# Optimization experiments

Measured on AMD Instinct MI355X. Metric: run time of the kernel, lower is better.

The kernel has to match this reference:

```python
import jax, jax.numpy as jnp
import numpy as np

H = 200  # LSTM units per layer
SEQ_LEN = 100
NUM_AXIS = 4


def setup_inputs() -> dict:
    key = jax.random.key(0)
    ks = jax.random.split(key, 12)
    B = 8192
    s = 0.05  # small init scale to avoid gate saturation
    inp = {
        "x": jax.random.normal(ks[0], (B, SEQ_LEN, 1), dtype=jnp.float32),
        # layer 0: input dim 1
        "W0": jax.random.normal(ks[1], (1, 4 * H), dtype=jnp.float32) * s,
        "U0": jax.random.normal(ks[2], (H, 4 * H), dtype=jnp.float32) * s,
        "b0": jax.random.normal(ks[3], (4 * H,), dtype=jnp.float32) * s,
        # layer 1
        "W1": jax.random.normal(ks[4], (H, 4 * H), dtype=jnp.float32) * s,
        "U1": jax.random.normal(ks[5], (H, 4 * H), dtype=jnp.float32) * s,
        "b1": jax.random.normal(ks[6], (4 * H,), dtype=jnp.float32) * s,
        # layer 2
        "W2": jax.random.normal(ks[7], (H, 4 * H), dtype=jnp.float32) * s,
        "U2": jax.random.normal(ks[8], (H, 4 * H), dtype=jnp.float32) * s,
        "b2": jax.random.normal(ks[9], (4 * H,), dtype=jnp.float32) * s,
        # dense head: 200 -> 400, tanh
        "Wfc": jax.random.normal(ks[10], (H, SEQ_LEN * NUM_AXIS), dtype=jnp.float32) * s,
        "bfc": jax.random.normal(ks[11], (SEQ_LEN * NUM_AXIS,), dtype=jnp.float32) * s,
    }
    return inp


def _lstm_step(h, c, xt, W, U, b):
    # Keras LSTMCell gate order: i, f, g(candidate), o
    z = xt @ W + h @ U + b  # [B, 4H]
    i, f, g, o = jnp.split(z, 4, axis=-1)
    c_new = jax.nn.sigmoid(f) * c + jax.nn.sigmoid(i) * jnp.tanh(g)
    h_new = jax.nn.sigmoid(o) * jnp.tanh(c_new)
    return h_new, c_new


def reference(x, W0, U0, b0, W1, U1, b1, W2, U2, b2, Wfc, bfc):
    B = x.shape[0]
    zeros = jnp.zeros((B, H), dtype=x.dtype)
    carry0 = (zeros, zeros, zeros, zeros, zeros, zeros)

    def step(carry, xt):
        h0, c0, h1, c1, h2, c2 = carry
        h0, c0 = _lstm_step(h0, c0, xt, W0, U0, b0)
        h1, c1 = _lstm_step(h1, c1, h0, W1, U1, b1)
        h2, c2 = _lstm_step(h2, c2, h1, W2, U2, b2)
        return (h0, c0, h1, c1, h2, c2), None

    # scan over time: x is [B, T, 1] -> [T, B, 1]
    xs = jnp.swapaxes(x, 0, 1)
    (h0, c0, h1, c1, h2, c2), _ = jax.lax.scan(step, carry0, xs)
    # return_sequences=False -> final top-layer hidden state
    y = jnp.tanh(h2 @ Wfc + bfc)  # [B, 400]
    return y.reshape(B, SEQ_LEN, NUM_AXIS)
```

## Files before the change

### kernel.cpp

```cpp
#include <hip/hip_runtime.h>

#define Hdim 200
#define NP   800
#define Tlen 100
#define BT   32
#define KB   7
#define HS   232
#define NT   50
#define THREADS 640
#define CH   5
#define CHSTR (NT*64*8)
#define MATSZ (KB*CHSTR)
#define SBUF  2560

#define WAIT_VM0   0x0F70
#define WAIT_VM5   0x0F75
#define WAIT_LGKM0 0xC07F

typedef float f32x4 __attribute__((ext_vector_type(4)));
typedef short s16x8 __attribute__((ext_vector_type(8)));

__device__ __forceinline__ ushort f2bf(float f) {
    unsigned u = __float_as_uint(f);
    return (ushort)((u + 0x7fffu + ((u >> 16) & 1u)) >> 16);
}
__device__ __forceinline__ float bf2f(ushort s) {
    return __uint_as_float(((unsigned)s) << 16);
}
__device__ __forceinline__ float sigmoid_fast(float v) {
    return 1.0f / (1.0f + __expf(-v));
}
__device__ __forceinline__ float tanh_fast(float v) {
    return 2.0f / (1.0f + __expf(-2.0f * v)) - 1.0f;
}
__device__ __forceinline__ void wg_barrier() {
    asm volatile("" ::: "memory");
    __builtin_amdgcn_s_waitcnt(WAIT_LGKM0);
    __builtin_amdgcn_s_barrier();
    asm volatile("" ::: "memory");
}

__global__ void pack_weights(const float* __restrict__ U0, const float* __restrict__ W1,
                             const float* __restrict__ U1, const float* __restrict__ W2,
                             const float* __restrict__ U2, ushort* __restrict__ dst) {
    int idx = blockIdx.x * blockDim.x + threadIdx.x;
    if (idx >= 5 * KB * NT * 64) return;
    int lane = idx & 63; int rest = idx >> 6;
    int nt = rest % NT; rest /= NT;
    int kb = rest % KB; int mi = rest / KB;
    const float* src = (mi == 0) ? U0 : (mi == 1) ? W1 : (mi == 2) ? U1 : (mi == 3) ? W2 : U2;
    int np = nt * 16 + (lane & 15);
    int ncol = (np & 3) * Hdim + (np >> 2);
    int k0 = kb * 32 + (lane >> 4) * 8;
    ushort v[8];
#pragma unroll
    for (int j = 0; j < 8; ++j) {
        int k = k0 + j;
        v[j] = (k < Hdim) ? f2bf(src[k * NP + ncol]) : (ushort)0;
    }
    uint4 o;
    o.x = (unsigned)v[0] | ((unsigned)v[1] << 16);
    o.y = (unsigned)v[2] | ((unsigned)v[3] << 16);
    o.z = (unsigned)v[4] | ((unsigned)v[5] << 16);
    o.w = (unsigned)v[6] | ((unsigned)v[7] << 16);
    ((uint4*)dst)[idx] = o;
}

__device__ __forceinline__ void stage_chunk(const ushort* gp, ushort* dstbuf, int lane) {
#pragma unroll
    for (int mt = 0; mt < CH; ++mt) {
        __builtin_amdgcn_global_load_lds(
            (const __attribute__((address_space(1))) void*)(gp + (size_t)mt * 512 + lane * 8),
            (__attribute__((address_space(3))) void*)(dstbuf + mt * 512),
            16, 0, 0);
    }
}

__device__ __forceinline__ void unpack4(const ushort* p, float (&o)[4]) {
    uint2 u = *(const uint2*)p;
    o[0] = bf2f((ushort)(u.x));  o[1] = bf2f((ushort)(u.x >> 16));
    o[2] = bf2f((ushort)(u.y));  o[3] = bf2f((ushort)(u.y >> 16));
}

__device__ __forceinline__ void gate_phase(f32x4 (&acc)[2][CH],
                                           float (&creg)[2][CH],
                                           ushort* __restrict__ hbl,
                                           int lane, int ct0) {
    const int l15 = lane & 15, q = lane >> 4;
#pragma unroll
    for (int nt = 0; nt < 2; ++nt) {
#pragma unroll
        for (int mt = 0; mt < CH; ++mt) {
            const int u = (ct0 + mt) * 4 + q;
            const int n = nt * 16 + l15;
            f32x4 z = acc[nt][mt];
            float iv = sigmoid_fast(z[0]);
            float fv = sigmoid_fast(z[1]);
            float gv = tanh_fast(z[2]);
            float ov = sigmoid_fast(z[3]);
            float c = fv * creg[nt][mt] + iv * gv;
            creg[nt][mt] = c;
            hbl[n * HS + u] = f2bf(ov * tanh_fast(c));
        }
    }
}

__global__ void __launch_bounds__(THREADS)
lstm3_mfma(const float* __restrict__ x,
           const float* __restrict__ W0, const float* __restrict__ b0,
           const float* __restrict__ b1, const float* __restrict__ b2,
           const float* __restrict__ Wfc, const float* __restrict__ bfc,
           const ushort* __restrict__ packed,
           float* __restrict__ out) {
    __shared__ ushort hb[3][BT][HS];
    __shared__ ushort stage[10][2][SBUF];
    __shared__ ushort pbwb[4][NP];
    __shared__ ushort xTs[Tlen][BT];
    __shared__ uint   gTab[35];
    __shared__ uint   bhTab[35];

    const int tid = threadIdx.x;
    const int wave = tid >> 6, lane = tid & 63;
    const int l15 = lane & 15, q = lane >> 4;
    const int ct0 = wave * CH;
    const int bx = blockIdx.x;
    const int bbase = bx * BT;

    for (int i = tid; i < 3 * BT * HS; i += THREADS) ((ushort*)hb)[i] = 0;
    for (int i = tid; i < NP; i += THREADS) {
        int nc = (i & 3) * Hdim + (i >> 2);
        pbwb[0][i] = f2bf(b0[nc]); pbwb[1][i] = f2bf(b1[nc]);
        pbwb[2][i] = f2bf(b2[nc]); pbwb[3][i] = f2bf(W0[nc]);
    }
    for (int i = tid; i < BT * Tlen; i += THREADS) {
        int m = i / Tlen, tt = i % Tlen;
        xTs[tt][m] = f2bf(x[(size_t)(bbase + m) * Tlen + tt]);
    }
    if (tid < 35) {
        int s = tid; uint goff, bhoff;
        if (s < 7) {
            int c = (s + bx) % 7;
            goff = 0u * MATSZ + c * CHSTR;           bhoff = 0u * BT * HS + c * 32;
        } else if (s < 21) {
            int c = (s - 7 + bx) % 14;
            if (c < 7) { goff = 2u * MATSZ + c * CHSTR;       bhoff = 1u * BT * HS + c * 32; }
            else       { goff = 1u * MATSZ + (c - 7) * CHSTR; bhoff = 0u * BT * HS + (c - 7) * 32; }
        } else {
            int c = (s - 21 + bx * 5) % 14;
            if (c < 7) { goff = 4u * MATSZ + c * CHSTR;       bhoff = 2u * BT * HS + c * 32; }
            else       { goff = 3u * MATSZ + (c - 7) * CHSTR; bhoff = 1u * BT * HS + (c - 7) * 32; }
        }
        gTab[s] = goff; bhTab[s] = bhoff;
    }
    __syncthreads();

    float creg[3][2][CH];
#pragma unroll
    for (int l = 0; l < 3; ++l)
#pragma unroll
        for (int nt = 0; nt < 2; ++nt)
#pragma unroll
            for (int mt = 0; mt < CH; ++mt) creg[l][nt][mt] = 0.0f;

    const ushort* pk = packed + (size_t)(ct0 * 64) * 8;
    ushort* sl = &stage[wave][0][0];
    ushort* hbflat = &hb[0][0][0];
    const int bhbase = l15 * HS + q * 8;

    stage_chunk(pk + gTab[0], sl, lane);
    stage_chunk(pk + gTab[1], sl + SBUF, lane);
    int isl = 2;

    for (int t = 0; t < Tlen; ++t) {
        f32x4 acc[2][CH];

        const float xn0 = bf2f(xTs[t][l15]);
        const float xn1 = bf2f(xTs[t][16 + l15]);
#pragma unroll
        for (int mt = 0; mt < CH; ++mt) {
            const int row = (ct0 + mt) * 16 + q * 4;
            float bb[4], ww[4];
            unpack4(&pbwb[0][row], bb);
            unpack4(&pbwb[3][row], ww);
#pragma unroll
            for (int r = 0; r < 4; ++r) {
                acc[0][mt][r] = fmaf(xn0, ww[r], bb[r]);
                acc[1][mt][r] = fmaf(xn1, ww[r], bb[r]);
            }
        }

#pragma unroll 1
        for (int s = 0; s < 7; ++s) {
            __builtin_amdgcn_s_waitcnt(WAIT_VM5);
            ushort* buf = sl + ((t + s) & 1) * SBUF;
            s16x8 frag[CH];
#pragma unroll
            for (int mt = 0; mt < CH; ++mt)
                frag[mt] = *(const s16x8*)(buf + mt * 512 + lane * 8);
            const ushort* bp = hbflat + bhTab[s] + bhbase;
            s16x8 bh0 = *(const s16x8*)bp;
            s16x8 bh1 = *(const s16x8*)(bp + 16 * HS);
#pragma unroll
            for (int mt = 0; mt < CH; ++mt) {
                acc[0][mt] = __builtin_amdgcn_mfma_f32_16x16x32_bf16(frag[mt], bh0, acc[0][mt], 0, 0, 0);
                acc[1][mt] = __builtin_amdgcn_mfma_f32_16x16x32_bf16(frag[mt], bh1, acc[1][mt], 0, 0, 0);
            }
            __builtin_amdgcn_s_waitcnt(WAIT_LGKM0);
            stage_chunk(pk + gTab[isl], buf, lane);
            isl = (isl == 34) ? 0 : isl + 1;
        }
        wg_barrier();
        gate_phase(acc, creg[0], hbflat + 0 * BT * HS, lane, ct0);
        wg_barrier();

#pragma unroll
        for (int mt = 0; mt < CH; ++mt) {
            const int row = (ct0 + mt) * 16 + q * 4;
            float bb[4];
            unpack4(&pbwb[1][row], bb);
#pragma unroll
            for (int r = 0; r < 4; ++r) { acc[0][mt][r] = bb[r]; acc[1][mt][r] = bb[r]; }
        }
#pragma unroll 1
        for (int s = 7; s < 21; ++s) {
            __builtin_amdgcn_s_waitcnt(WAIT_VM5);
            ushort* buf = sl + ((t + s) & 1) * SBUF;
            s16x8 frag[CH];
#pragma unroll
            for (int mt = 0; mt < CH; ++mt)
                frag[mt] = *(const s16x8*)(buf + mt * 512 + lane * 8);
            const ushort* bp = hbflat + bhTab[s] + bhbase;
            s16x8 bh0 = *(const s16x8*)bp;
            s16x8 bh1 = *(const s16x8*)(bp + 16 * HS);
#pragma unroll
            for (int mt = 0; mt < CH; ++mt) {
                acc[0][mt] = __builtin_amdgcn_mfma_f32_16x16x32_bf16(frag[mt], bh0, acc[0][mt], 0, 0, 0);
                acc[1][mt] = __builtin_amdgcn_mfma_f32_16x16x32_bf16(frag[mt], bh1, acc[1][mt], 0, 0, 0);
            }
            __builtin_amdgcn_s_waitcnt(WAIT_LGKM0);
            stage_chunk(pk + gTab[isl], buf, lane);
            isl = (isl == 34) ? 0 : isl + 1;
        }
        wg_barrier();
        gate_phase(acc, creg[1], hbflat + 1 * BT * HS, lane, ct0);
        wg_barrier();

#pragma unroll
        for (int mt = 0; mt < CH; ++mt) {
            const int row = (ct0 + mt) * 16 + q * 4;
            float bb[4];
            unpack4(&pbwb[2][row], bb);
#pragma unroll
            for (int r = 0; r < 4; ++r) { acc[0][mt][r] = bb[r]; acc[1][mt][r] = bb[r]; }
        }
#pragma unroll 1
        for (int s = 21; s < 35; ++s) {
            __builtin_amdgcn_s_waitcnt(WAIT_VM5);
            ushort* buf = sl + ((t + s) & 1) * SBUF;
            s16x8 frag[CH];
#pragma unroll
            for (int mt = 0; mt < CH; ++mt)
                frag[mt] = *(const s16x8*)(buf + mt * 512 + lane * 8);
            const ushort* bp = hbflat + bhTab[s] + bhbase;
            s16x8 bh0 = *(const s16x8*)bp;
            s16x8 bh1 = *(const s16x8*)(bp + 16 * HS);
#pragma unroll
            for (int mt = 0; mt < CH; ++mt) {
                acc[0][mt] = __builtin_amdgcn_mfma_f32_16x16x32_bf16(frag[mt], bh0, acc[0][mt], 0, 0, 0);
                acc[1][mt] = __builtin_amdgcn_mfma_f32_16x16x32_bf16(frag[mt], bh1, acc[1][mt], 0, 0, 0);
            }
            __builtin_amdgcn_s_waitcnt(WAIT_LGKM0);
            stage_chunk(pk + gTab[isl], buf, lane);
            isl = (isl == 34) ? 0 : isl + 1;
        }
        wg_barrier();
        gate_phase(acc, creg[2], hbflat + 2 * BT * HS, lane, ct0);
        wg_barrier();
    }
    __syncthreads();

    for (int gidx = tid; gidx < BT * 100; gidx += THREADS) {
        int m = gidx / 100;
        int j4 = (gidx % 100) * 4;
        const ushort* h2 = &hb[2][m][0];
        float4 a4 = *(const float4*)(bfc + j4);
        float s0 = a4.x, s1 = a4.y, s2 = a4.z, s3 = a4.w;
        for (int k = 0; k < Hdim; ++k) {
            float hk = bf2f(h2[k]);
            float4 w4 = *(const float4*)(Wfc + (size_t)k * 400 + j4);
            s0 = fmaf(hk, w4.x, s0);
            s1 = fmaf(hk, w4.y, s1);
            s2 = fmaf(hk, w4.z, s2);
            s3 = fmaf(hk, w4.w, s3);
        }
        float4 o4;
        o4.x = tanh_fast(s0); o4.y = tanh_fast(s1);
        o4.z = tanh_fast(s2); o4.w = tanh_fast(s3);
        *(float4*)(out + (size_t)(bbase + m) * 400 + j4) = o4;
    }
}

extern "C" void kernel_launch(void* const* d_in, const int* in_sizes, int n_in,
                              void* d_out, int out_size, void* d_ws, size_t ws_size,
                              hipStream_t stream) {
    const float* x   = (const float*)d_in[0];
    const float* W0  = (const float*)d_in[1];
    const float* U0  = (const float*)d_in[2];
    const float* b0  = (const float*)d_in[3];
    const float* W1  = (const float*)d_in[4];
    const float* U1  = (const float*)d_in[5];
    const float* b1  = (const float*)d_in[6];
    const float* W2  = (const float*)d_in[7];
    const float* U2  = (const float*)d_in[8];
    const float* b2  = (const float*)d_in[9];
    const float* Wfc = (const float*)d_in[10];
    const float* bfc = (const float*)d_in[11];
    float* out = (float*)d_out;
    ushort* packed = (ushort*)d_ws;

    const int B = in_sizes[0] / Tlen;
    const int pack_threads = 5 * KB * NT * 64;
    pack_weights<<<(pack_threads + 255) / 256, 256, 0, stream>>>(U0, W1, U1, W2, U2, packed);
    lstm3_mfma<<<B / BT, THREADS, 0, stream>>>(x, W0, b0, b1, b2, Wfc, bfc, packed, out);
}
```

Measured before the change: 2.800 ms.

## Reorder LSTM matmul chunks to drop post-gate barriers per layer

Reorders the staged weight chunks so that each layer first multiplies against the hidden state of the layer whose fresh value is not yet needed. A barrier then sits between the two halves instead of after each gate phase, removing three workgroup barriers per timestep. The intent is to overlap the recurrent half of each matmul with other waves finishing their gate phase. It relies on careful reasoning about read-after-write hazards on the shared hidden buffers, which are now protected only by the reordered barriers.

Measured after the change: 2.840 ms. About the same (+1.4%).

```diff
diff --git a/kernel.cpp b/kernel.cpp
--- a/kernel.cpp
+++ b/kernel.cpp
@@ -13,7 +13,6 @@
 #define MATSZ (KB*CHSTR)
 #define SBUF  2560
 
-#define WAIT_VM0   0x0F70
 #define WAIT_VM5   0x0F75
 #define WAIT_LGKM0 0xC07F
 
@@ -82,6 +81,35 @@
     o[2] = bf2f((ushort)(u.y));  o[3] = bf2f((ushort)(u.y >> 16));
 }
 
+template<int S0, int S1>
+__device__ __forceinline__ void do_region(f32x4 (&acc)[2][CH],
+                                          const ushort* __restrict__ pk, ushort* sl,
+                                          const uint* __restrict__ gTab,
+                                          const uint* __restrict__ bhTab,
+                                          const ushort* __restrict__ hbflat,
+                                          int bhbase, int lane, int t, int& isl) {
+#pragma unroll 1
+    for (int s = S0; s < S1; ++s) {
+        __builtin_amdgcn_s_waitcnt(WAIT_VM5);
+        ushort* buf = sl + ((t + s) & 1) * SBUF;
+        s16x8 frag[CH];
+#pragma unroll
+        for (int mt = 0; mt < CH; ++mt)
+            frag[mt] = *(const s16x8*)(buf + mt * 512 + lane * 8);
+        const ushort* bp = hbflat + bhTab[s] + bhbase;
+        s16x8 bh0 = *(const s16x8*)bp;
+        s16x8 bh1 = *(const s16x8*)(bp + 16 * HS);
+#pragma unroll
+        for (int mt = 0; mt < CH; ++mt) {
+            acc[0][mt] = __builtin_amdgcn_mfma_f32_16x16x32_bf16(frag[mt], bh0, acc[0][mt], 0, 0, 0);
+            acc[1][mt] = __builtin_amdgcn_mfma_f32_16x16x32_bf16(frag[mt], bh1, acc[1][mt], 0, 0, 0);
+        }
+        __builtin_amdgcn_s_waitcnt(WAIT_LGKM0);
+        stage_chunk(pk + gTab[isl], buf, lane);
+        isl = (isl == 34) ? 0 : isl + 1;
+    }
+}
+
 __device__ __forceinline__ void gate_phase(f32x4 (&acc)[2][CH],
                                            float (&creg)[2][CH],
                                            ushort* __restrict__ hbl,
@@ -137,19 +165,13 @@
         xTs[tt][m] = f2bf(x[(size_t)(bbase + m) * Tlen + tt]);
     }
     if (tid < 35) {
-        int s = tid; uint goff, bhoff;
-        if (s < 7) {
-            int c = (s + bx) % 7;
-            goff = 0u * MATSZ + c * CHSTR;           bhoff = 0u * BT * HS + c * 32;
-        } else if (s < 21) {
-            int c = (s - 7 + bx) % 14;
-            if (c < 7) { goff = 2u * MATSZ + c * CHSTR;       bhoff = 1u * BT * HS + c * 32; }
-            else       { goff = 1u * MATSZ + (c - 7) * CHSTR; bhoff = 0u * BT * HS + (c - 7) * 32; }
-        } else {
-            int c = (s - 21 + bx * 5) % 14;
-            if (c < 7) { goff = 4u * MATSZ + c * CHSTR;       bhoff = 2u * BT * HS + c * 32; }
-            else       { goff = 3u * MATSZ + (c - 7) * CHSTR; bhoff = 1u * BT * HS + (c - 7) * 32; }
-        }
+        int s = tid; int r = s % 7; int c = (r + bx) % 7;
+        uint goff, bhoff;
+        if (s < 7)       { goff = 0u * MATSZ + c * CHSTR; bhoff = 0u * BT * HS + c * 32; }
+        else if (s < 14) { goff = 2u * MATSZ + c * CHSTR; bhoff = 1u * BT * HS + c * 32; }
+        else if (s < 21) { goff = 1u * MATSZ + c * CHSTR; bhoff = 0u * BT * HS + c * 32; }
+        else if (s < 28) { goff = 4u * MATSZ + c * CHSTR; bhoff = 2u * BT * HS + c * 32; }
+        else             { goff = 3u * MATSZ + c * CHSTR; bhoff = 1u * BT * HS + c * 32; }
         gTab[s] = goff; bhTab[s] = bhoff;
     }
     __syncthreads();
@@ -188,30 +210,9 @@
                 acc[1][mt][r] = fmaf(xn1, ww[r], bb[r]);
             }
         }
-
-#pragma unroll 1
-        for (int s = 0; s < 7; ++s) {
-            __builtin_amdgcn_s_waitcnt(WAIT_VM5);
-            ushort* buf = sl + ((t + s) & 1) * SBUF;
-            s16x8 frag[CH];
-#pragma unroll
-            for (int mt = 0; mt < CH; ++mt)
-                frag[mt] = *(const s16x8*)(buf + mt * 512 + lane * 8);
-            const ushort* bp = hbflat + bhTab[s] + bhbase;
-            s16x8 bh0 = *(const s16x8*)bp;
-            s16x8 bh1 = *(const s16x8*)(bp + 16 * HS);
-#pragma unroll
-            for (int mt = 0; mt < CH; ++mt) {
-                acc[0][mt] = __builtin_amdgcn_mfma_f32_16x16x32_bf16(frag[mt], bh0, acc[0][mt], 0, 0, 0);
-                acc[1][mt] = __builtin_amdgcn_mfma_f32_16x16x32_bf16(frag[mt], bh1, acc[1][mt], 0, 0, 0);
-            }
-            __builtin_amdgcn_s_waitcnt(WAIT_LGKM0);
-            stage_chunk(pk + gTab[isl], buf, lane);
-            isl = (isl == 34) ? 0 : isl + 1;
-        }
+        do_region<0, 7>(acc, pk, sl, gTab, bhTab, hbflat, bhbase, lane, t, isl);
         wg_barrier();
         gate_phase(acc, creg[0], hbflat + 0 * BT * HS, lane, ct0);
-        wg_barrier();
 
 #pragma unroll
         for (int mt = 0; mt < CH; ++mt) {
@@ -221,29 +222,10 @@
 #pragma unroll
             for (int r = 0; r < 4; ++r) { acc[0][mt][r] = bb[r]; acc[1][mt][r] = bb[r]; }
         }
-#pragma unroll 1
-        for (int s = 7; s < 21; ++s) {
-            __builtin_amdgcn_s_waitcnt(WAIT_VM5);
-            ushort* buf = sl + ((t + s) & 1) * SBUF;
-            s16x8 frag[CH];
-#pragma unroll
-            for (int mt = 0; mt < CH; ++mt)
-                frag[mt] = *(const s16x8*)(buf + mt * 512 + lane * 8);
-            const ushort* bp = hbflat + bhTab[s] + bhbase;
-            s16x8 bh0 = *(const s16x8*)bp;
-            s16x8 bh1 = *(const s16x8*)(bp + 16 * HS);
-#pragma unroll
-            for (int mt = 0; mt < CH; ++mt) {
-                acc[0][mt] = __builtin_amdgcn_mfma_f32_16x16x32_bf16(frag[mt], bh0, acc[0][mt], 0, 0, 0);
-                acc[1][mt] = __builtin_amdgcn_mfma_f32_16x16x32_bf16(frag[mt], bh1, acc[1][mt], 0, 0, 0);
-            }
-            __builtin_amdgcn_s_waitcnt(WAIT_LGKM0);
-            stage_chunk(pk + gTab[isl], buf, lane);
-            isl = (isl == 34) ? 0 : isl + 1;
-        }
+        do_region<7, 14>(acc, pk, sl, gTab, bhTab, hbflat, bhbase, lane, t, isl);
         wg_barrier();
+        do_region<14, 21>(acc, pk, sl, gTab, bhTab, hbflat, bhbase, lane, t, isl);
         gate_phase(acc, creg[1], hbflat + 1 * BT * HS, lane, ct0);
-        wg_barrier();
 
 #pragma unroll
         for (int mt = 0; mt < CH; ++mt) {
@@ -253,29 +235,10 @@
 #pragma unroll
             for (int r = 0; r < 4; ++r) { acc[0][mt][r] = bb[r]; acc[1][mt][r] = bb[r]; }
         }
-#pragma unroll 1
-        for (int s = 21; s < 35; ++s) {
-            __builtin_amdgcn_s_waitcnt(WAIT_VM5);
-            ushort* buf = sl + ((t + s) & 1) * SBUF;
-            s16x8 frag[CH];
-#pragma unroll
-            for (int mt = 0; mt < CH; ++mt)
-                frag[mt] = *(const s16x8*)(buf + mt * 512 + lane * 8);
-            const ushort* bp = hbflat + bhTab[s] + bhbase;
-            s16x8 bh0 = *(const s16x8*)bp;
-            s16x8 bh1 = *(const s16x8*)(bp + 16 * HS);
-#pragma unroll
-            for (int mt = 0; mt < CH; ++mt) {
-                acc[0][mt] = __builtin_amdgcn_mfma_f32_16x16x32_bf16(frag[mt], bh0, acc[0][mt], 0, 0, 0);
-                acc[1][mt] = __builtin_amdgcn_mfma_f32_16x16x32_bf16(frag[mt], bh1, acc[1][mt], 0, 0, 0);
-            }
-            __builtin_amdgcn_s_waitcnt(WAIT_LGKM0);
-            stage_chunk(pk + gTab[isl], buf, lane);
-            isl = (isl == 34) ? 0 : isl + 1;
-        }
+        do_region<21, 28>(acc, pk, sl, gTab, bhTab, hbflat, bhbase, lane, t, isl);
         wg_barrier();
+        do_region<28, 35>(acc, pk, sl, gTab, bhTab, hbflat, bhbase, lane, t, isl);
         gate_phase(acc, creg[2], hbflat + 2 * BT * HS, lane, ct0);
-        wg_barrier();
     }
     __syncthreads();
 
```
